# Kernel optimization log

Hardware: AMD Instinct MI355X
Metric: run time of the kernel (lower is better)

## Reference

```python
import jax, jax.numpy as jnp
import numpy as np

N = 50000
E = 800000
IN_C = 128
HID = 32
HEADS = 4
G = 512      # number of graphs in batch
OUT_C = 100
NEG_SLOPE = 0.2
EPS = 1e-16


def _gat_params(key, f_in, heads, c):
    k1, k2, k3, k4 = jax.random.split(key, 4)
    s = 1.0 / np.sqrt(f_in)
    return {
        'W': jax.random.uniform(k1, (heads * c, f_in), jnp.float32, -s, s),
        'att_src': jax.random.normal(k2, (heads, c), jnp.float32) * 0.1,
        'att_dst': jax.random.normal(k3, (heads, c), jnp.float32) * 0.1,
        'b': jnp.zeros((heads * c,), jnp.float32),
    }


def setup_inputs() -> dict:
    key = jax.random.key(0)
    ks = jax.random.split(key, 8)
    x = jax.random.normal(ks[0], (N, IN_C), jnp.float32)
    edge_index = jax.random.randint(ks[1], (2, E), 0, N, jnp.int64)
    batch = jnp.sort(jax.random.randint(ks[2], (N,), 0, G, jnp.int64))
    p1 = _gat_params(ks[3], IN_C, HEADS, HID)
    p2 = _gat_params(ks[4], HEADS * HID, HEADS, HID)
    p3 = _gat_params(ks[5], HEADS * HID, HEADS, HID)
    s = 1.0 / np.sqrt(HEADS * HID)
    fc_W = jax.random.uniform(ks[6], (OUT_C, HEADS * HID), jnp.float32, -s, s)
    fc_b = jnp.zeros((OUT_C,), jnp.float32)
    return {
        'x': x, 'edge_index': edge_index, 'batch': batch,
        'W1': p1['W'], 'as1': p1['att_src'], 'ad1': p1['att_dst'], 'b1': p1['b'],
        'W2': p2['W'], 'as2': p2['att_src'], 'ad2': p2['att_dst'], 'b2': p2['b'],
        'W3': p3['W'], 'as3': p3['att_src'], 'ad3': p3['att_dst'], 'b3': p3['b'],
        'fc_W': fc_W, 'fc_b': fc_b,
    }


def gat_conv(x, src, dst, W, att_src, att_dst, b):
    # x: [N, F_in] -> h: [N, H, C]
    h = (x @ W.T).reshape(N, HEADS, HID)
    a_src = jnp.einsum('nhc,hc->nh', h, att_src)   # [N, H]
    a_dst = jnp.einsum('nhc,hc->nh', h, att_dst)
    alpha = a_src[src] + a_dst[dst]                 # [E', H]
    alpha = jax.nn.leaky_relu(alpha, NEG_SLOPE)
    # segment softmax over incoming edges of each dst node
    m = jax.ops.segment_max(alpha, dst, num_segments=N)
    alpha = jnp.exp(alpha - m[dst])
    denom = jax.ops.segment_sum(alpha, dst, num_segments=N)
    alpha = alpha / (denom[dst] + EPS)
    msg = alpha[:, :, None] * h[src]                # [E', H, C]
    out = jax.ops.segment_sum(msg, dst, num_segments=N)
    return out.reshape(N, HEADS * HID) + b


def reference(x, edge_index, batch,
              W1, as1, ad1, b1, W2, as2, ad2, b2, W3, as3, ad3, b3,
              fc_W, fc_b):
    # add self loops (PyG GATConv default)
    loops = jnp.arange(N, dtype=edge_index.dtype)
    src = jnp.concatenate([edge_index[0], loops])
    dst = jnp.concatenate([edge_index[1], loops])
    h = jax.nn.elu(gat_conv(x, src, dst, W1, as1, ad1, b1))
    h = jax.nn.elu(gat_conv(h, src, dst, W2, as2, ad2, b2))
    h = jax.nn.elu(gat_conv(h, src, dst, W3, as3, ad3, b3))
    # global mean pool over graphs
    sums = jax.ops.segment_sum(h, batch, num_segments=G)        # [G, H*C]
    cnts = jax.ops.segment_sum(jnp.ones((N,), h.dtype), batch, num_segments=G)
    pooled = sums / jnp.maximum(cnts, 1.0)[:, None]
    # dropout p=0.5 is identity in eval mode
    return pooled @ fc_W.T + fc_b
```

## Files before the change

kernel.cpp:

```cpp
#include <hip/hip_runtime.h>
#include <math.h>

#define NN 50000
#define EE 800000
#define GG 512
#define OUTC 100
#define NEG 0.2f
#define STRIDE 64
#define NPART 8
#define PRNG (NN / NPART)
#define PCHUNK 4096
#define SCAT_BLOCKS (NPART * 196)

typedef __attribute__((ext_vector_type(8))) short bf16x8;
typedef __attribute__((ext_vector_type(8))) short s16x8;
typedef __attribute__((ext_vector_type(8))) unsigned short us8;
typedef __attribute__((ext_vector_type(4))) float f32x4;

__device__ inline ushort f2bf(float v) {
  unsigned u = __float_as_uint(v);
  unsigned r = (u + 0x7fff + ((u >> 16) & 1)) >> 16;
  return (ushort)r;
}

__global__ __launch_bounds__(256) void k_scatter_prep(const int* __restrict__ ei,
    int* __restrict__ cursor, ushort* __restrict__ srcs,
    const float* __restrict__ W0, const float* __restrict__ W1, const float* __restrict__ W2,
    const float* __restrict__ as0, const float* __restrict__ as1, const float* __restrict__ as2,
    const float* __restrict__ ad0, const float* __restrict__ ad1, const float* __restrict__ ad2,
    ushort* __restrict__ hi, ushort* __restrict__ lo) {
  if (blockIdx.x < SCAT_BLOCKS) {
    int part = blockIdx.x & (NPART - 1);
    int chunk = blockIdx.x >> 3;
    int plo = part * PRNG, phi = plo + PRNG;
    int base = chunk * PCHUNK;
    for (int i = threadIdx.x; i < PCHUNK; i += 256) {
      int e = base + i;
      if (e >= EE) break;
      int d = ei[EE + e];
      if (d < plo || d >= phi) continue;
      int s = ei[e];
      int pos = atomicAdd(&cursor[d], 1);
      if (pos < STRIDE) srcs[(d << 6) + pos] = (ushort)s;
    }
  } else {
    int pb = blockIdx.x - SCAT_BLOCKS;
    int layer = pb / 68, bx = pb % 68;
    const float* W  = (layer == 0) ? W0 : (layer == 1) ? W1 : W2;
    const float* av = (layer == 0) ? as0 : (layer == 1) ? as1 : as2;
    const float* dv = (layer == 0) ? ad0 : (layer == 1) ? ad1 : ad2;
    ushort* hiL = hi + (size_t)layer * 144 * 128;
    ushort* loL = lo + (size_t)layer * 144 * 128;
    int idx = bx * 256 + threadIdx.x;
    if (bx < 64) {
      float v = W[idx];
      ushort hb = f2bf(v);
      float hf = __uint_as_float(((unsigned)hb) << 16);
      hiL[idx] = hb;
      loL[idx] = f2bf(v - hf);
    } else {
      int j2 = idx - 64 * 256;
      int j = j2 >> 7, k = j2 & 127;
      int head = j & 3;
      const float* vec = (j < 4) ? &av[head * 32] : &dv[head * 32];
      float dot = 0.f;
#pragma unroll
      for (int c = 0; c < 32; c++) dot += W[(head * 32 + c) * 128 + k] * vec[c];
      ushort hb = f2bf(dot);
      float hf = __uint_as_float(((unsigned)hb) << 16);
      hiL[(128 + j) * 128 + k] = hb;
      loL[(128 + j) * 128 + k] = f2bf(dot - hf);
      hiL[(136 + j) * 128 + k] = 0;
      loL[(136 + j) * 128 + k] = 0;
    }
  }
}

template <bool TAIL>
__device__ __forceinline__ void gemm_core(const float* __restrict__ feat,
    const ushort* __restrict__ Whi, const ushort* __restrict__ Wlo,
    short* __restrict__ hq, float* __restrict__ scalef,
    float* __restrict__ asrcf, float* __restrict__ adstf, int n0, int t) {
  int wave = t >> 6, lane = t & 63;
  int quad = lane >> 4, r16 = lane & 15;

  f32x4 acc[2][9];
#pragma unroll
  for (int mt = 0; mt < 2; mt++)
#pragma unroll
    for (int nt = 0; nt < 9; nt++) acc[mt][nt] = (f32x4)0.f;

#pragma unroll
  for (int ks = 0; ks < 4; ks++) {
    bf16x8 ah[2], al[2];
#pragma unroll
    for (int mt = 0; mt < 2; mt++) {
      int row = n0 + wave * 32 + mt * 16 + r16;
      float4 va, vb;
      if (TAIL && row >= NN) {
        va = make_float4(0.f, 0.f, 0.f, 0.f); vb = va;
      } else {
        const float4* fp = (const float4*)&feat[(size_t)row * 128 + ks * 32 + quad * 8];
        va = fp[0]; vb = fp[1];
      }
      float vv[8] = {va.x, va.y, va.z, va.w, vb.x, vb.y, vb.z, vb.w};
      us8 hh, ll;
#pragma unroll
      for (int j = 0; j < 8; j++) {
        ushort hb = f2bf(vv[j]);
        float hf = __uint_as_float(((unsigned)hb) << 16);
        hh[j] = hb;
        ll[j] = (ushort)(__float_as_uint(vv[j] - hf) >> 16);
      }
      ah[mt] = (bf16x8)hh;
      al[mt] = (bf16x8)ll;
    }
#pragma unroll
    for (int nt = 0; nt < 9; nt++) {
      int wrow = (nt < 8) ? (nt * 16 + r16) : (128 + r16);
      size_t wo = (size_t)wrow * 128 + ks * 32 + quad * 8;
      bf16x8 bh = *(const bf16x8*)&Whi[wo];
      bf16x8 bl = *(const bf16x8*)&Wlo[wo];
#pragma unroll
      for (int mt = 0; mt < 2; mt++) {
        acc[mt][nt] = __builtin_amdgcn_mfma_f32_16x16x32_bf16(ah[mt], bh, acc[mt][nt], 0, 0, 0);
        acc[mt][nt] = __builtin_amdgcn_mfma_f32_16x16x32_bf16(al[mt], bh, acc[mt][nt], 0, 0, 0);
        acc[mt][nt] = __builtin_amdgcn_mfma_f32_16x16x32_bf16(ah[mt], bl, acc[mt][nt], 0, 0, 0);
      }
    }
  }

#pragma unroll
  for (int mt = 0; mt < 2; mt++) {
#pragma unroll
    for (int reg = 0; reg < 4; reg++) {
      float am = 0.f;
#pragma unroll
      for (int nt = 0; nt < 8; nt++) am = fmaxf(am, fabsf(acc[mt][nt][reg]));
#pragma unroll
      for (int off = 1; off < 16; off <<= 1) am = fmaxf(am, __shfl_xor(am, off));
      int node = n0 + wave * 32 + mt * 16 + quad * 4 + reg;
      if (!TAIL || node < NN) {
        float amc = fmaxf(am, 1e-20f);
        float rq = 32767.f / amc;
        if (r16 == 0) scalef[node] = amc * (1.f / 32767.f);
        if (r16 < 4) asrcf[node * 4 + r16] = acc[mt][8][reg];
        else if (r16 < 8) adstf[node * 4 + r16 - 4] = acc[mt][8][reg];
        short* dq = &hq[(size_t)node * 128 + r16];
#pragma unroll
        for (int nt = 0; nt < 8; nt++)
          dq[nt * 16] = (short)__float2int_rn(acc[mt][nt][reg] * rq);
      }
    }
  }
}

__global__ __launch_bounds__(256) void k_gemm_mfma(const float* __restrict__ feat,
    const ushort* __restrict__ Whi, const ushort* __restrict__ Wlo,
    short* __restrict__ hq, float* __restrict__ scalef,
    float* __restrict__ asrcf, float* __restrict__ adstf) {
  int n0 = blockIdx.x * 128;
  if (n0 + 128 <= NN)
    gemm_core<false>(feat, Whi, Wlo, hq, scalef, asrcf, adstf, n0, threadIdx.x);
  else
    gemm_core<true>(feat, Whi, Wlo, hq, scalef, asrcf, adstf, n0, threadIdx.x);
}

__global__ __launch_bounds__(256) void k_gather(const short* __restrict__ hq,
    const float* __restrict__ scalef,
    const float4* __restrict__ asrc, const float4* __restrict__ adst,
    const int* __restrict__ cursor, const ushort* __restrict__ srcs,
    const float* __restrict__ bias, float* __restrict__ outf) {
  __shared__ int s_src[4][4][16];
  __shared__ float s_w[4][4][72];
  __shared__ float s_e[4][4][72];

  int wave = threadIdx.x >> 6, lane = threadIdx.x & 63;
  int grp = lane >> 4;
  int gl = lane & 15;
  int node = blockIdx.x * 16 + wave * 4 + grp;

  int deg = 0, e0 = 0;
  float4 ad = make_float4(0.f, 0.f, 0.f, 0.f);
  if (node < NN) {
    deg = min(cursor[node], STRIDE);
    e0 = node << 6;
    ad = adst[node];
  }
  int c0 = gl << 3;
  int head = gl >> 2;

  float acc[8];
#pragma unroll
  for (int i = 0; i < 8; i++) acc[i] = 0.f;
  float wsum = 0.f;

  if (node < NN) {
    float4 a = asrc[node];
    float sc = scalef[node];
    float v, w0, w1, w2, w3;
    v = a.x + ad.x; v = v > 0.f ? v : NEG * v; w0 = expf(v);
    v = a.y + ad.y; v = v > 0.f ? v : NEG * v; w1 = expf(v);
    v = a.z + ad.z; v = v > 0.f ? v : NEG * v; w2 = expf(v);
    v = a.w + ad.w; v = v > 0.f ? v : NEG * v; w3 = expf(v);
    float wh = (head == 0) ? w0 : (head == 1) ? w1 : (head == 2) ? w2 : w3;
    wsum = wh;
    float ws = wh * sc;
    s16x8 qs = *(const s16x8*)&hq[(node << 7) + c0];
#pragma unroll
    for (int i = 0; i < 8; i++) acc[i] = ws * (float)qs[i];
  }

  int rounds = (deg + 15) >> 4;
  for (int r = 0; r < rounds; r++) {
    int base = r << 4;
    int j = base + gl;
    int sn = 0;
    float w0 = 0.f, w1 = 0.f, w2 = 0.f, w3 = 0.f, sc = 0.f;
    if (j < deg) {
      sn = srcs[e0 + j];
      float4 a = asrc[sn];
      sc = scalef[sn];
      float v;
      v = a.x + ad.x; v = v > 0.f ? v : NEG * v; w0 = expf(v);
      v = a.y + ad.y; v = v > 0.f ? v : NEG * v; w1 = expf(v);
      v = a.z + ad.z; v = v > 0.f ? v : NEG * v; w2 = expf(v);
      v = a.w + ad.w; v = v > 0.f ? v : NEG * v; w3 = expf(v);
    }
    s_src[wave][grp][gl] = sn << 7;
    float* wp = &s_w[wave][grp][gl << 2];
    wp[0] = w0 * sc; wp[1] = w1 * sc; wp[2] = w2 * sc; wp[3] = w3 * sc;
    float* ep = &s_e[wave][grp][gl << 2];
    ep[0] = w0; ep[1] = w1; ep[2] = w2; ep[3] = w3;

    int cnt = min(16, deg - base);
    int cntp = (cnt + 3) & ~3;
    for (int k = 0; k < cntp; k += 4) {
      int ra = s_src[wave][grp][k + 0];
      int rb = s_src[wave][grp][k + 1];
      int rc = s_src[wave][grp][k + 2];
      int rd = s_src[wave][grp][k + 3];
      float wa = s_w[wave][grp][((k + 0) << 2) | head];
      float wb = s_w[wave][grp][((k + 1) << 2) | head];
      float wc = s_w[wave][grp][((k + 2) << 2) | head];
      float wd = s_w[wave][grp][((k + 3) << 2) | head];
      wsum += s_e[wave][grp][((k + 0) << 2) | head]
            + s_e[wave][grp][((k + 1) << 2) | head]
            + s_e[wave][grp][((k + 2) << 2) | head]
            + s_e[wave][grp][((k + 3) << 2) | head];
      s16x8 qa = *(const s16x8*)&hq[ra + c0];
      s16x8 qb = *(const s16x8*)&hq[rb + c0];
      s16x8 qc = *(const s16x8*)&hq[rc + c0];
      s16x8 qd = *(const s16x8*)&hq[rd + c0];
#pragma unroll
      for (int i = 0; i < 8; i++) acc[i] = fmaf(wa, (float)qa[i], acc[i]);
#pragma unroll
      for (int i = 0; i < 8; i++) acc[i] = fmaf(wb, (float)qb[i], acc[i]);
#pragma unroll
      for (int i = 0; i < 8; i++) acc[i] = fmaf(wc, (float)qc[i], acc[i]);
#pragma unroll
      for (int i = 0; i < 8; i++) acc[i] = fmaf(wd, (float)qd[i], acc[i]);
    }
  }

  if (node < NN) {
    float rcp = 1.f / (wsum + 1e-16f);
    float o[8];
#pragma unroll
    for (int i = 0; i < 8; i++) {
      float v = acc[i] * rcp + bias[c0 + i];
      o[i] = v > 0.f ? v : expm1f(v);
    }
    *(float4*)&outf[(size_t)node * 128 + c0] = make_float4(o[0], o[1], o[2], o[3]);
    *(float4*)&outf[(size_t)node * 128 + c0 + 4] = make_float4(o[4], o[5], o[6], o[7]);
  }
}

__global__ __launch_bounds__(128) void k_pool(const float* __restrict__ feat,
    const int* __restrict__ batch, float* __restrict__ pooled, float* __restrict__ cnt) {
  int n0 = blockIdx.x * 32;
  int c = threadIdx.x;
  float acc = 0.f; int curg = -1;
  for (int i = 0; i < 32; i++) {
    int n = n0 + i;
    if (n >= NN) break;
    int g = batch[n];
    if (g != curg) {
      if (curg >= 0) atomicAdd(&pooled[curg * 128 + c], acc);
      acc = 0.f; curg = g;
    }
    acc += feat[n * 128 + c];
  }
  if (curg >= 0) atomicAdd(&pooled[curg * 128 + c], acc);
  if (threadIdx.x == 0) {
    float cc = 0.f; int cg = -1;
    for (int i = 0; i < 32; i++) {
      int n = n0 + i;
      if (n >= NN) break;
      int g = batch[n];
      if (g != cg) { if (cg >= 0) atomicAdd(&cnt[cg], cc); cc = 0.f; cg = g; }
      cc += 1.f;
    }
    if (cg >= 0) atomicAdd(&cnt[cg], cc);
  }
}

__global__ __launch_bounds__(128) void k_fc(const float* __restrict__ pooled,
    const float* __restrict__ cnt, const float* __restrict__ fcW,
    const float* __restrict__ fcb, float* __restrict__ out) {
  int g = blockIdx.x;
  __shared__ float p[128];
  int t = threadIdx.x;
  float inv = 1.0f / fmaxf(cnt[g], 1.0f);
  p[t] = pooled[g * 128 + t] * inv;
  __syncthreads();
  if (t < OUTC) {
    float acc = fcb[t];
    const float4* wr = (const float4*)&fcW[t * 128];
    const float4* pp = (const float4*)p;
#pragma unroll
    for (int i = 0; i < 32; i++) {
      float4 w = wr[i], pv = pp[i];
      acc = fmaf(w.x, pv.x, fmaf(w.y, pv.y, fmaf(w.z, pv.z, fmaf(w.w, pv.w, acc))));
    }
    out[g * OUTC + t] = acc;
  }
}

extern "C" void kernel_launch(void* const* d_in, const int* in_sizes, int n_in,
                              void* d_out, int out_size, void* d_ws, size_t ws_size,
                              hipStream_t stream) {
  const float* x    = (const float*)d_in[0];
  const int*   ei   = (const int*)d_in[1];
  const int*   batch= (const int*)d_in[2];
  const float* W1   = (const float*)d_in[3];
  const float* as1  = (const float*)d_in[4];
  const float* ad1  = (const float*)d_in[5];
  const float* b1   = (const float*)d_in[6];
  const float* W2   = (const float*)d_in[7];
  const float* as2  = (const float*)d_in[8];
  const float* ad2  = (const float*)d_in[9];
  const float* b2   = (const float*)d_in[10];
  const float* W3   = (const float*)d_in[11];
  const float* as3  = (const float*)d_in[12];
  const float* ad3  = (const float*)d_in[13];
  const float* b3   = (const float*)d_in[14];
  const float* fcW  = (const float*)d_in[15];
  const float* fcb  = (const float*)d_in[16];
  float* out = (float*)d_out;

  char* p = (char*)d_ws;
  auto alloc = [&](size_t bytes) { char* r = p; p += (bytes + 255) & ~(size_t)255; return r; };
  short* hq     = (short*)alloc((size_t)NN * 128 * 2);
  float* scalef = (float*)alloc((size_t)NN * 4);
  float* buf0   = (float*)alloc((size_t)NN * 128 * 4);
  float* asrc   = (float*)alloc((size_t)NN * 4 * 4);
  float* adst   = (float*)alloc((size_t)NN * 4 * 4);
  char*  zbase  = p;
  int*   cursor = (int*)alloc((size_t)NN * 4);
  float* pooled = (float*)alloc((size_t)GG * 128 * 4);
  float* cnt    = (float*)alloc((size_t)GG * 4);
  size_t zlen   = (size_t)(p - zbase);
  ushort* srcs  = (ushort*)alloc((size_t)NN * STRIDE * 2);
  ushort* whi   = (ushort*)alloc((size_t)3 * 144 * 128 * 2);
  ushort* wlo   = (ushort*)alloc((size_t)3 * 144 * 128 * 2);

  hipMemsetAsync(zbase, 0, zlen, stream);

  k_scatter_prep<<<SCAT_BLOCKS + 204, 256, 0, stream>>>(ei, cursor, srcs,
      W1, W2, W3, as1, as2, as3, ad1, ad2, ad3, whi, wlo);

  const float* bs[3] = {b1, b2, b3};
  const float* fin = x;
  for (int l = 0; l < 3; l++) {
    k_gemm_mfma<<<(NN + 127) / 128, 256, 0, stream>>>(fin,
        whi + (size_t)l * 144 * 128, wlo + (size_t)l * 144 * 128,
        hq, scalef, asrc, adst);
    k_gather<<<(NN + 15) / 16, 256, 0, stream>>>(hq, scalef,
        (const float4*)asrc, (const float4*)adst,
        cursor, srcs, bs[l], buf0);
    fin = buf0;
  }
  k_pool<<<(NN + 31) / 32, 128, 0, stream>>>(buf0, batch, pooled, cnt);
  k_fc<<<GG, 128, 0, stream>>>(pooled, cnt, fcW, fcb, out);
}
```

Measured before the change: 362.4 us.

## Double-buffer gather rounds, pack asrc with scale, simplify edge scatter

Edge scatter drops the 8-way destination partitioning and lets each block process 1024 edges directly, which cuts redundant reads of the edge list but loses locality of the atomic updates. The per-node source attention and quantization scale now share one 32-byte record, so each gathered neighbor needs one fetch instead of two. The gather kernel double-buffers its shared-memory edge metadata so the next round's source loads overlap the current round's row accumulation. It also moves the softmax denominator into per-lane register sums reduced by shuffles, uses fast __expf, and reads up to 8 neighbor rows at once.

```diff
diff --git a/kernel.cpp b/kernel.cpp
--- a/kernel.cpp
+++ b/kernel.cpp
@@ -7,10 +7,7 @@
 #define OUTC 100
 #define NEG 0.2f
 #define STRIDE 64
-#define NPART 8
-#define PRNG (NN / NPART)
-#define PCHUNK 4096
-#define SCAT_BLOCKS (NPART * 196)
+#define SCAT_BLOCKS 782
 
 typedef __attribute__((ext_vector_type(8))) short bf16x8;
 typedef __attribute__((ext_vector_type(8))) short s16x8;
@@ -30,18 +27,16 @@
     const float* __restrict__ ad0, const float* __restrict__ ad1, const float* __restrict__ ad2,
     ushort* __restrict__ hi, ushort* __restrict__ lo) {
   if (blockIdx.x < SCAT_BLOCKS) {
-    int part = blockIdx.x & (NPART - 1);
-    int chunk = blockIdx.x >> 3;
-    int plo = part * PRNG, phi = plo + PRNG;
-    int base = chunk * PCHUNK;
-    for (int i = threadIdx.x; i < PCHUNK; i += 256) {
-      int e = base + i;
-      if (e >= EE) break;
-      int d = ei[EE + e];
-      if (d < plo || d >= phi) continue;
-      int s = ei[e];
-      int pos = atomicAdd(&cursor[d], 1);
-      if (pos < STRIDE) srcs[(d << 6) + pos] = (ushort)s;
+    int base = blockIdx.x << 10;
+#pragma unroll
+    for (int t = 0; t < 4; ++t) {
+      int e = base + (t << 8) + threadIdx.x;
+      if (e < EE) {
+        int d = ei[EE + e];
+        int s = ei[e];
+        int pos = atomicAdd(&cursor[d], 1);
+        if (pos < STRIDE) srcs[(d << 6) + pos] = (ushort)s;
+      }
     }
   } else {
     int pb = blockIdx.x - SCAT_BLOCKS;
@@ -79,8 +74,8 @@
 template <bool TAIL>
 __device__ __forceinline__ void gemm_core(const float* __restrict__ feat,
     const ushort* __restrict__ Whi, const ushort* __restrict__ Wlo,
-    short* __restrict__ hq, float* __restrict__ scalef,
-    float* __restrict__ asrcf, float* __restrict__ adstf, int n0, int t) {
+    short* __restrict__ hq, float* __restrict__ asp,
+    float* __restrict__ adstf, int n0, int t) {
   int wave = t >> 6, lane = t & 63;
   int quad = lane >> 4, r16 = lane & 15;
 
@@ -143,9 +138,9 @@
       if (!TAIL || node < NN) {
         float amc = fmaxf(am, 1e-20f);
         float rq = 32767.f / amc;
-        if (r16 == 0) scalef[node] = amc * (1.f / 32767.f);
-        if (r16 < 4) asrcf[node * 4 + r16] = acc[mt][8][reg];
+        if (r16 < 4) asp[node * 8 + r16] = acc[mt][8][reg];
         else if (r16 < 8) adstf[node * 4 + r16 - 4] = acc[mt][8][reg];
+        else if (r16 == 8) asp[node * 8 + 4] = amc * (1.f / 32767.f);
         short* dq = &hq[(size_t)node * 128 + r16];
 #pragma unroll
         for (int nt = 0; nt < 8; nt++)
@@ -157,28 +152,29 @@
 
 __global__ __launch_bounds__(256) void k_gemm_mfma(const float* __restrict__ feat,
     const ushort* __restrict__ Whi, const ushort* __restrict__ Wlo,
-    short* __restrict__ hq, float* __restrict__ scalef,
-    float* __restrict__ asrcf, float* __restrict__ adstf) {
+    short* __restrict__ hq, float* __restrict__ asp,
+    float* __restrict__ adstf) {
   int n0 = blockIdx.x * 128;
   if (n0 + 128 <= NN)
-    gemm_core<false>(feat, Whi, Wlo, hq, scalef, asrcf, adstf, n0, threadIdx.x);
+    gemm_core<false>(feat, Whi, Wlo, hq, asp, adstf, n0, threadIdx.x);
   else
-    gemm_core<true>(feat, Whi, Wlo, hq, scalef, asrcf, adstf, n0, threadIdx.x);
+    gemm_core<true>(feat, Whi, Wlo, hq, asp, adstf, n0, threadIdx.x);
 }
 
 __global__ __launch_bounds__(256) void k_gather(const short* __restrict__ hq,
-    const float* __restrict__ scalef,
-    const float4* __restrict__ asrc, const float4* __restrict__ adst,
+    const float* __restrict__ asp,
+    const float4* __restrict__ adst,
     const int* __restrict__ cursor, const ushort* __restrict__ srcs,
     const float* __restrict__ bias, float* __restrict__ outf) {
-  __shared__ int s_src[4][4][16];
-  __shared__ float s_w[4][4][72];
-  __shared__ float s_e[4][4][72];
+  __shared__ alignas(16) int   s_src[2][4][4][16];
+  __shared__ alignas(16) float s_wt[2][4][4][4][20];
 
   int wave = threadIdx.x >> 6, lane = threadIdx.x & 63;
   int grp = lane >> 4;
   int gl = lane & 15;
   int node = blockIdx.x * 16 + wave * 4 + grp;
+  int head = gl >> 2;
+  int c0 = gl << 3;
 
   int deg = 0, e0 = 0;
   float4 ad = make_float4(0.f, 0.f, 0.f, 0.f);
@@ -187,88 +183,131 @@
     e0 = node << 6;
     ad = adst[node];
   }
-  int c0 = gl << 3;
-  int head = gl >> 2;
+  int rounds = (deg + 15) >> 4;
 
   float acc[8];
 #pragma unroll
   for (int i = 0; i < 8; i++) acc[i] = 0.f;
-  float wsum = 0.f;
+  float ws0 = 0.f, ws1 = 0.f, ws2 = 0.f, ws3 = 0.f;
+  float wself = 0.f;
+
+  int nsn = 0, nlive = 0;
+
+  auto phase1 = [&](int r) {
+    int j = (r << 4) + gl;
+    nlive = (j < deg);
+    nsn = nlive ? (int)srcs[e0 + j] : 0;
+  };
+
+  auto phase2 = [&](int b) {
+    float q0 = 0.f, q1 = 0.f, q2 = 0.f, q3 = 0.f;
+    if (nlive) {
+      const float4 a = *(const float4*)&asp[nsn * 8];
+      float sc = asp[nsn * 8 + 4];
+      float v, w0, w1, w2, w3;
+      v = a.x + ad.x; v = v > 0.f ? v : NEG * v; w0 = __expf(v);
+      v = a.y + ad.y; v = v > 0.f ? v : NEG * v; w1 = __expf(v);
+      v = a.z + ad.z; v = v > 0.f ? v : NEG * v; w2 = __expf(v);
+      v = a.w + ad.w; v = v > 0.f ? v : NEG * v; w3 = __expf(v);
+      ws0 += w0; ws1 += w1; ws2 += w2; ws3 += w3;
+      q0 = w0 * sc; q1 = w1 * sc; q2 = w2 * sc; q3 = w3 * sc;
+    }
+    s_src[b][wave][grp][gl] = nsn << 7;
+    s_wt[b][wave][grp][0][gl] = q0;
+    s_wt[b][wave][grp][1][gl] = q1;
+    s_wt[b][wave][grp][2][gl] = q2;
+    s_wt[b][wave][grp][3][gl] = q3;
+  };
+
+  auto consume = [&](int r, int b) {
+    int cnt = deg - (r << 4);
+    cnt = min(cnt, 16);
+    const int* srow = &s_src[b][wave][grp][0];
+    const float* wrow = &s_wt[b][wave][grp][head][0];
+#pragma unroll
+    for (int c = 0; c < 2; ++c) {
+      int k0 = c << 3;
+      if (k0 < cnt) {
+        int4 sa = *(const int4*)&srow[k0];
+        int4 sb = *(const int4*)&srow[k0 + 4];
+        float4 wa = *(const float4*)&wrow[k0];
+        float4 wb = *(const float4*)&wrow[k0 + 4];
+        s16x8 qa = *(const s16x8*)&hq[sa.x + c0];
+        s16x8 qb = *(const s16x8*)&hq[sa.y + c0];
+        s16x8 qc = *(const s16x8*)&hq[sa.z + c0];
+        s16x8 qd = *(const s16x8*)&hq[sa.w + c0];
+        s16x8 qe = *(const s16x8*)&hq[sb.x + c0];
+        s16x8 qf = *(const s16x8*)&hq[sb.y + c0];
+        s16x8 qg = *(const s16x8*)&hq[sb.z + c0];
+        s16x8 qh = *(const s16x8*)&hq[sb.w + c0];
+#pragma unroll
+        for (int i = 0; i < 8; i++) acc[i] = fmaf(wa.x, (float)qa[i], acc[i]);
+#pragma unroll
+        for (int i = 0; i < 8; i++) acc[i] = fmaf(wa.y, (float)qb[i], acc[i]);
+#pragma unroll
+        for (int i = 0; i < 8; i++) acc[i] = fmaf(wa.z, (float)qc[i], acc[i]);
+#pragma unroll
+        for (int i = 0; i < 8; i++) acc[i] = fmaf(wa.w, (float)qd[i], acc[i]);
+        if (k0 + 4 < cnt) {
+#pragma unroll
+          for (int i = 0; i < 8; i++) acc[i] = fmaf(wb.x, (float)qe[i], acc[i]);
+#pragma unroll
+          for (int i = 0; i < 8; i++) acc[i] = fmaf(wb.y, (float)qf[i], acc[i]);
+#pragma unroll
+          for (int i = 0; i < 8; i++) acc[i] = fmaf(wb.z, (float)qg[i], acc[i]);
+#pragma unroll
+          for (int i = 0; i < 8; i++) acc[i] = fmaf(wb.w, (float)qh[i], acc[i]);
+        }
+      }
+    }
+  };
+
+  phase1(0);
 
   if (node < NN) {
-    float4 a = asrc[node];
-    float sc = scalef[node];
+    const float4 a = *(const float4*)&asp[node * 8];
+    float sc = asp[node * 8 + 4];
     float v, w0, w1, w2, w3;
-    v = a.x + ad.x; v = v > 0.f ? v : NEG * v; w0 = expf(v);
-    v = a.y + ad.y; v = v > 0.f ? v : NEG * v; w1 = expf(v);
-    v = a.z + ad.z; v = v > 0.f ? v : NEG * v; w2 = expf(v);
-    v = a.w + ad.w; v = v > 0.f ? v : NEG * v; w3 = expf(v);
+    v = a.x + ad.x; v = v > 0.f ? v : NEG * v; w0 = __expf(v);
+    v = a.y + ad.y; v = v > 0.f ? v : NEG * v; w1 = __expf(v);
+    v = a.z + ad.z; v = v > 0.f ? v : NEG * v; w2 = __expf(v);
+    v = a.w + ad.w; v = v > 0.f ? v : NEG * v; w3 = __expf(v);
     float wh = (head == 0) ? w0 : (head == 1) ? w1 : (head == 2) ? w2 : w3;
-    wsum = wh;
-    float ws = wh * sc;
+    wself = wh;
+    float wssc = wh * sc;
     s16x8 qs = *(const s16x8*)&hq[(node << 7) + c0];
 #pragma unroll
-    for (int i = 0; i < 8; i++) acc[i] = ws * (float)qs[i];
-  }
-
-  int rounds = (deg + 15) >> 4;
-  for (int r = 0; r < rounds; r++) {
-    int base = r << 4;
-    int j = base + gl;
-    int sn = 0;
-    float w0 = 0.f, w1 = 0.f, w2 = 0.f, w3 = 0.f, sc = 0.f;
-    if (j < deg) {
-      sn = srcs[e0 + j];
-      float4 a = asrc[sn];
-      sc = scalef[sn];
-      float v;
-      v = a.x + ad.x; v = v > 0.f ? v : NEG * v; w0 = expf(v);
-      v = a.y + ad.y; v = v > 0.f ? v : NEG * v; w1 = expf(v);
-      v = a.z + ad.z; v = v > 0.f ? v : NEG * v; w2 = expf(v);
-      v = a.w + ad.w; v = v > 0.f ? v : NEG * v; w3 = expf(v);
-    }
-    s_src[wave][grp][gl] = sn << 7;
-    float* wp = &s_w[wave][grp][gl << 2];
-    wp[0] = w0 * sc; wp[1] = w1 * sc; wp[2] = w2 * sc; wp[3] = w3 * sc;
-    float* ep = &s_e[wave][grp][gl << 2];
-    ep[0] = w0; ep[1] = w1; ep[2] = w2; ep[3] = w3;
-
-    int cnt = min(16, deg - base);
-    int cntp = (cnt + 3) & ~3;
-    for (int k = 0; k < cntp; k += 4) {
-      int ra = s_src[wave][grp][k + 0];
-      int rb = s_src[wave][grp][k + 1];
-      int rc = s_src[wave][grp][k + 2];
-      int rd = s_src[wave][grp][k + 3];
-      float wa = s_w[wave][grp][((k + 0) << 2) | head];
-      float wb = s_w[wave][grp][((k + 1) << 2) | head];
-      float wc = s_w[wave][grp][((k + 2) << 2) | head];
-      float wd = s_w[wave][grp][((k + 3) << 2) | head];
-      wsum += s_e[wave][grp][((k + 0) << 2) | head]
-            + s_e[wave][grp][((k + 1) << 2) | head]
-            + s_e[wave][grp][((k + 2) << 2) | head]
-            + s_e[wave][grp][((k + 3) << 2) | head];
-      s16x8 qa = *(const s16x8*)&hq[ra + c0];
-      s16x8 qb = *(const s16x8*)&hq[rb + c0];
-      s16x8 qc = *(const s16x8*)&hq[rc + c0];
-      s16x8 qd = *(const s16x8*)&hq[rd + c0];
-#pragma unroll
-      for (int i = 0; i < 8; i++) acc[i] = fmaf(wa, (float)qa[i], acc[i]);
-#pragma unroll
-      for (int i = 0; i < 8; i++) acc[i] = fmaf(wb, (float)qb[i], acc[i]);
-#pragma unroll
-      for (int i = 0; i < 8; i++) acc[i] = fmaf(wc, (float)qc[i], acc[i]);
-#pragma unroll
-      for (int i = 0; i < 8; i++) acc[i] = fmaf(wd, (float)qd[i], acc[i]);
-    }
+    for (int i = 0; i < 8; i++) acc[i] = wssc * (float)qs[i];
+  }
+
+  if (rounds > 0) {
+    phase2(0);
+    for (int r = 0; r < rounds; ++r) {
+      int b = r & 1;
+      if (r + 1 < rounds) phase1(r + 1);
+      consume(r, b);
+      if (r + 1 < rounds) phase2(b ^ 1);
+    }
+  }
+
+#pragma unroll
+  for (int off = 1; off < 16; off <<= 1) {
+    ws0 += __shfl_xor(ws0, off);
+    ws1 += __shfl_xor(ws1, off);
+    ws2 += __shfl_xor(ws2, off);
+    ws3 += __shfl_xor(ws3, off);
   }
 
   if (node < NN) {
+    float wsum = wself + ((head == 0) ? ws0 : (head == 1) ? ws1 : (head == 2) ? ws2 : ws3);
     float rcp = 1.f / (wsum + 1e-16f);
+    float4 bv0 = *(const float4*)&bias[c0];
+    float4 bv1 = *(const float4*)&bias[c0 + 4];
+    float bb[8] = {bv0.x, bv0.y, bv0.z, bv0.w, bv1.x, bv1.y, bv1.z, bv1.w};
     float o[8];
 #pragma unroll
     for (int i = 0; i < 8; i++) {
-      float v = acc[i] * rcp + bias[c0 + i];
+      float v = acc[i] * rcp + bb[i];
       o[i] = v > 0.f ? v : expm1f(v);
     }
     *(float4*)&outf[(size_t)node * 128 + c0] = make_float4(o[0], o[1], o[2], o[3]);
@@ -352,10 +391,9 @@
   char* p = (char*)d_ws;
   auto alloc = [&](size_t bytes) { char* r = p; p += (bytes + 255) & ~(size_t)255; return r; };
   short* hq     = (short*)alloc((size_t)NN * 128 * 2);
-  float* scalef = (float*)alloc((size_t)NN * 4);
+  float* asp    = (float*)alloc((size_t)NN * 8 * 4);
   float* buf0   = (float*)alloc((size_t)NN * 128 * 4);
-  float* asrc   = (float*)alloc((size_t)NN * 4 * 4);
-  float* adst   = (float*)alloc((size_t)NN * 4 * 4);
+  float* adstv  = (float*)alloc((size_t)NN * 4 * 4);
   char*  zbase  = p;
   int*   cursor = (int*)alloc((size_t)NN * 4);
   float* pooled = (float*)alloc((size_t)GG * 128 * 4);
@@ -375,10 +413,9 @@
   for (int l = 0; l < 3; l++) {
     k_gemm_mfma<<<(NN + 127) / 128, 256, 0, stream>>>(fin,
         whi + (size_t)l * 144 * 128, wlo + (size_t)l * 144 * 128,
-        hq, scalef, asrc, adst);
-    k_gather<<<(NN + 15) / 16, 256, 0, stream>>>(hq, scalef,
-        (const float4*)asrc, (const float4*)adst,
-        cursor, srcs, bs[l], buf0);
+        hq, asp, adstv);
+    k_gather<<<(NN + 15) / 16, 256, 0, stream>>>(hq, asp,
+        (const float4*)adstv, cursor, srcs, bs[l], buf0);
     fin = buf0;
   }
   k_pool<<<(NN + 31) / 32, 128, 0, stream>>>(buf0, batch, pooled, cnt);
```

Measured after the change: 375.9 us. 3.7% more time.
